# Optimization experiments

Measured on AMD Instinct MI355X. Metric: run time of the kernel, lower is better.

## Reference

```python
import jax, jax.numpy as jnp
import numpy as np

N, NFEAT, NHID, NCLASS, NHEADS = 50000, 512, 256, 64, 8
C1 = NHID // NHEADS  # 32 per-head channels, layer 1
NEG_SLOPE = 0.2


def setup_inputs() -> dict:
    key = jax.random.key(0)
    ks = jax.random.split(key, 10)
    x = jax.random.normal(ks[0], (N, NFEAT), dtype=jnp.float32)
    edge_idx = jax.random.randint(ks[1], (2, 800000), 0, N, dtype=jnp.int64)
    s = 0.05
    return {
        "x": x,
        "edge_idx": edge_idx,
        "W1": jax.random.normal(ks[2], (NFEAT, NHEADS, C1), dtype=jnp.float32) * s,
        "a1_src": jax.random.normal(ks[3], (NHEADS, C1), dtype=jnp.float32) * s,
        "a1_dst": jax.random.normal(ks[4], (NHEADS, C1), dtype=jnp.float32) * s,
        "b1": jnp.zeros((NHID,), dtype=jnp.float32),
        "W2": jax.random.normal(ks[5], (NHID, NHEADS, NCLASS), dtype=jnp.float32) * s,
        "a2_src": jax.random.normal(ks[6], (NHEADS, NCLASS), dtype=jnp.float32) * s,
        "a2_dst": jax.random.normal(ks[7], (NHEADS, NCLASS), dtype=jnp.float32) * s,
        "b2": jnp.zeros((NCLASS,), dtype=jnp.float32),
    }


def gat_conv(x, src, dst, W, a_src, a_dst, b, concat):
    # x: [N, F_in]; W: [F_in, H, C]; a_*: [H, C]; src/dst: [E]
    h = jnp.einsum("nf,fhc->nhc", x, W)             # [N, H, C]
    e_src = jnp.sum(h * a_src, axis=-1)              # [N, H]
    e_dst = jnp.sum(h * a_dst, axis=-1)              # [N, H]
    alpha = e_src[src] + e_dst[dst]                  # [E, H]
    alpha = jnp.where(alpha > 0, alpha, NEG_SLOPE * alpha)  # leaky_relu(0.2)
    # segment softmax over incoming edges of each destination node
    m = jax.ops.segment_max(alpha, dst, num_segments=N)     # [N, H]
    m = jnp.where(jnp.isfinite(m), m, 0.0)
    e = jnp.exp(alpha - m[dst])                      # [E, H]
    z = jax.ops.segment_sum(e, dst, num_segments=N)  # [N, H]
    coef = e / z[dst]                                # [E, H]
    msg = h[src] * coef[:, :, None]                  # [E, H, C]
    out = jax.ops.segment_sum(msg, dst, num_segments=N)  # [N, H, C]
    if concat:
        out = out.reshape(N, -1)
    else:
        out = out.mean(axis=1)
    return out + b


def reference(x, edge_idx, W1, a1_src, a1_dst, b1, W2, a2_src, a2_dst, b2):
    # add self loops (PyG GATConv default)
    loop = jnp.arange(N, dtype=edge_idx.dtype)
    src = jnp.concatenate([edge_idx[0], loop])
    dst = jnp.concatenate([edge_idx[1], loop])
    h = gat_conv(x, src, dst, W1, a1_src, a1_dst, b1, concat=True)   # [N, NHID]
    h = jax.nn.relu(h)
    # dropout inactive (eval mode)
    out = gat_conv(h, src, dst, W2, a2_src, a2_dst, b2, concat=False)  # [N, NCLASS]
    return jax.nn.log_softmax(out, axis=1)
```

## Files before the change

kernel.cpp:

```cpp
#include <hip/hip_runtime.h>
#include <math.h>

#define NN 50000
#define NF 512
#define NHID 256
#define NCLASS 64
#define NHEADS 8

typedef __attribute__((ext_vector_type(8))) short bf16x8;
typedef __attribute__((ext_vector_type(4))) float f32x4;
typedef __attribute__((ext_vector_type(2))) float f32x2;
typedef __attribute__((ext_vector_type(4))) unsigned int u32x4;
typedef __attribute__((ext_vector_type(2))) unsigned int u32x2;

static __device__ __forceinline__ unsigned short f2bf(float f) {
  unsigned int u = __float_as_uint(f);
  unsigned int r = (u + 0x7fffu + ((u >> 16) & 1u)) >> 16;
  return (unsigned short)r;
}
static __device__ __forceinline__ float bf2f(unsigned short u) {
  return __uint_as_float(((unsigned int)u) << 16);
}
static __device__ __forceinline__ float2 bfpair(unsigned int u) {
  return make_float2(__uint_as_float(u << 16), __uint_as_float(u & 0xffff0000u));
}

static __device__ __forceinline__ u32x4 gld128(const void* p) {
  u32x4 r;
  asm volatile("global_load_dwordx4 %0, %1, off"
               : "=v"(r) : "v"((unsigned long long)p));
  return r;
}
static __device__ __forceinline__ u32x2 gld64(const void* p) {
  u32x2 r;
  asm volatile("global_load_dwordx2 %0, %1, off"
               : "=v"(r) : "v"((unsigned long long)p));
  return r;
}
static __device__ __forceinline__ int gld32i(const void* p) {
  int r;
  asm volatile("global_load_dword %0, %1, off"
               : "=v"(r) : "v"((unsigned long long)p));
  return r;
}
static __device__ __forceinline__ float gld32f(const void* p) {
  float r;
  asm volatile("global_load_dword %0, %1, off"
               : "=v"(r) : "v"((unsigned long long)p));
  return r;
}
#define VMCNT0()                                        \
  do {                                                  \
    asm volatile("s_waitcnt vmcnt(0)" ::: "memory");    \
    __builtin_amdgcn_sched_barrier(0);                  \
  } while (0)

__global__ void k_init_deg(int* deg) {
  int i = blockIdx.x * blockDim.x + threadIdx.x;
  if (i < NN) deg[i] = 1;
}

__global__ void k_count(const int* __restrict__ dst, int E0, int* deg) {
  int i = blockIdx.x * blockDim.x + threadIdx.x;
  if (i < E0) atomicAdd(&deg[dst[i]], 1);
}

__global__ __launch_bounds__(1024) void k_scan(const int* __restrict__ deg, int* offs,
                                               int* cursor) {
  __shared__ int wbase[16];
  __shared__ int srun;
  int tid = threadIdx.x;
  int lane = tid & 63;
  int wv = tid >> 6;
  if (tid == 0) srun = 0;
  __syncthreads();
  for (int base = 0; base < NN; base += 4096) {
    int i = base + tid * 4;
    int4 v;
    if (i + 3 < NN) {
      v = *(const int4*)(deg + i);
    } else {
      v.x = (i + 0 < NN) ? deg[i + 0] : 0;
      v.y = (i + 1 < NN) ? deg[i + 1] : 0;
      v.z = (i + 2 < NN) ? deg[i + 2] : 0;
      v.w = (i + 3 < NN) ? deg[i + 3] : 0;
    }
    int tot = v.x + v.y + v.z + v.w;
    int s = tot;
    #pragma unroll
    for (int o = 1; o < 64; o <<= 1) {
      int t = __shfl_up(s, o);
      if (lane >= o) s += t;
    }
    if (lane == 63) wbase[wv] = s;
    __syncthreads();
    if (tid == 0) {
      int run = srun;
      #pragma unroll
      for (int w2 = 0; w2 < 16; w2++) {
        int t = wbase[w2];
        wbase[w2] = run;
        run += t;
      }
      srun = run;
    }
    __syncthreads();
    int p = wbase[wv] + s - tot;
    if (i + 0 < NN) { offs[i + 0] = p; cursor[i + 0] = p; p += v.x; }
    if (i + 1 < NN) { offs[i + 1] = p; cursor[i + 1] = p; p += v.y; }
    if (i + 2 < NN) { offs[i + 2] = p; cursor[i + 2] = p; p += v.z; }
    if (i + 3 < NN) { offs[i + 3] = p; cursor[i + 3] = p; }
  }
  __syncthreads();
  if (tid == 0) offs[NN] = srun;
}

__global__ void k_scatter(const int* __restrict__ src, const int* __restrict__ dst,
                          int E0, int* cursor, int* __restrict__ nbr) {
  int i = blockIdx.x * blockDim.x + threadIdx.x;
  if (i < E0) {
    int pos = atomicAdd(&cursor[dst[i]], 1);
    nbr[pos] = src[i];
  } else if (i < E0 + NN) {
    int v = i - E0;
    int pos = atomicAdd(&cursor[v], 1);
    nbr[pos] = v;
  }
}

__global__ void k_cast4(const float* __restrict__ in, unsigned short* __restrict__ out,
                        int n4) {
  int i = blockIdx.x * blockDim.x + threadIdx.x;
  if (i >= n4) return;
  float4 v = *(const float4*)(in + (size_t)i * 4);
  ushort4 o;
  o.x = f2bf(v.x); o.y = f2bf(v.y); o.z = f2bf(v.z); o.w = f2bf(v.w);
  *(ushort4*)(out + (size_t)i * 4) = o;
}

__global__ void k_castWt(const float* __restrict__ W, unsigned short* __restrict__ Wt,
                         int K, int cols) {
  int i = blockIdx.x * blockDim.x + threadIdx.x;
  if (i >= K * cols) return;
  int k = i / cols, c = i % cols;
  Wt[(size_t)c * K + k] = f2bf(W[i]);
}

__global__ void k_castWt_perm(const float* __restrict__ W, unsigned short* __restrict__ Wt,
                              int K) {
  int i = blockIdx.x * blockDim.x + threadIdx.x;
  if (i >= K * NHEADS * NCLASS) return;
  int k = i / (NHEADS * NCLASS);
  int rem = i % (NHEADS * NCLASS);
  int h = rem / NCLASS, c = rem % NCLASS;
  Wt[(size_t)(c * NHEADS + h) * K + k] = f2bf(W[i]);
}

__global__ void k_cast_fp8(const unsigned short* __restrict__ in,
                           unsigned char* __restrict__ out, int n8) {
  int i = blockIdx.x * blockDim.x + threadIdx.x;
  if (i >= n8) return;
  uint4 raw = *(const uint4*)(in + (size_t)i * 8);
  float2 p0 = bfpair(raw.x), p1 = bfpair(raw.y), p2 = bfpair(raw.z), p3 = bfpair(raw.w);
  int lo = 0, hi = 0;
  lo = __builtin_amdgcn_cvt_pk_fp8_f32(p0.x, p0.y, lo, false);
  lo = __builtin_amdgcn_cvt_pk_fp8_f32(p1.x, p1.y, lo, true);
  hi = __builtin_amdgcn_cvt_pk_fp8_f32(p2.x, p2.y, hi, false);
  hi = __builtin_amdgcn_cvt_pk_fp8_f32(p3.x, p3.y, hi, true);
  u32x2 o; o[0] = (unsigned int)lo; o[1] = (unsigned int)hi;
  *(u32x2*)(out + (size_t)i * 8) = o;
}

__global__ __launch_bounds__(256) void k_gemm_bf(const unsigned short* __restrict__ A,
                                                 const unsigned short* __restrict__ Bt,
                                                 unsigned short* __restrict__ C,
                                                 int rows, int K, int cols) {
  __shared__ unsigned short Bs[256 * 40];
  int t = threadIdx.x;
  int wave = t >> 6, lane = t & 63;
  int quad = lane >> 4, sixt = lane & 15;
  int rb = blockIdx.x * 64 + (wave >> 1) * 32;
  int cw = (wave & 1) * 128;
  int cbw = blockIdx.y * 256 + cw;
  int r0 = rb + sixt, r1 = rb + 16 + sixt;
  const unsigned short* Ap0 = A + (size_t)(r0 < rows ? r0 : 0) * K + quad * 8;
  const unsigned short* Ap1 = A + (size_t)(r1 < rows ? r1 : 0) * K + quad * 8;
  const unsigned short* Bg = Bt + (size_t)(blockIdx.y * 256 + (t >> 2)) * K + (t & 3) * 8;
  const size_t BgStep = (size_t)64 * K;
  char* BsW = (char*)Bs + (t >> 2) * 80 + (t & 3) * 16;
  f32x4 acc0[8] = {}, acc1[8] = {};
  for (int k0 = 0; k0 < K; k0 += 32) {
    uint4 v0 = *(const uint4*)(Bg + k0);
    uint4 v1 = *(const uint4*)(Bg + BgStep + k0);
    uint4 v2 = *(const uint4*)(Bg + 2 * BgStep + k0);
    uint4 v3 = *(const uint4*)(Bg + 3 * BgStep + k0);
    bf16x8 a0 = *(const bf16x8*)(Ap0 + k0);
    bf16x8 a1 = *(const bf16x8*)(Ap1 + k0);
    *(uint4*)(BsW) = v0;
    *(uint4*)(BsW + 64 * 80) = v1;
    *(uint4*)(BsW + 128 * 80) = v2;
    *(uint4*)(BsW + 192 * 80) = v3;
    __syncthreads();
    #pragma unroll
    for (int g = 0; g < 8; g++) {
      bf16x8 b = *(const bf16x8*)((const char*)Bs + (cw + g * 16 + sixt) * 80 + quad * 16);
      acc0[g] = __builtin_amdgcn_mfma_f32_16x16x32_bf16(a0, b, acc0[g], 0, 0, 0);
      acc1[g] = __builtin_amdgcn_mfma_f32_16x16x32_bf16(a1, b, acc1[g], 0, 0, 0);
    }
    __syncthreads();
  }
  #pragma unroll
  for (int r = 0; r < 4; r++) {
    int row = rb + quad * 4 + r;
    if (row < rows) {
      unsigned short* out = C + (size_t)row * cols + cbw + sixt;
      #pragma unroll
      for (int g = 0; g < 8; g++) out[g * 16] = f2bf(acc0[g][r]);
    }
    int row2 = row + 16;
    if (row2 < rows) {
      unsigned short* out = C + (size_t)row2 * cols + cbw + sixt;
      #pragma unroll
      for (int g = 0; g < 8; g++) out[g * 16] = f2bf(acc1[g][r]);
    }
  }
}

template <int C>
__global__ void k_escore_c(const unsigned short* __restrict__ h,
                           const float* __restrict__ asr, const float* __restrict__ ads,
                           float* __restrict__ es, float* __restrict__ ed) {
  int idx = blockIdx.x * blockDim.x + threadIdx.x;
  if (idx >= NN * NHEADS) return;
  int hd = idx & 7;
  const unsigned short* row = h + (size_t)idx * C;
  float s = 0.f, d = 0.f;
  #pragma unroll
  for (int c8 = 0; c8 < C / 8; c8++) {
    uint4 raw = *(const uint4*)(row + c8 * 8);
    float2 p0 = bfpair(raw.x), p1 = bfpair(raw.y), p2 = bfpair(raw.z), p3 = bfpair(raw.w);
    const float* as_ = asr + hd * C + c8 * 8;
    const float* ad_ = ads + hd * C + c8 * 8;
    s += p0.x * as_[0] + p0.y * as_[1] + p1.x * as_[2] + p1.y * as_[3] +
         p2.x * as_[4] + p2.y * as_[5] + p3.x * as_[6] + p3.y * as_[7];
    d += p0.x * ad_[0] + p0.y * ad_[1] + p1.x * ad_[2] + p1.y * ad_[3] +
         p2.x * ad_[4] + p2.y * ad_[5] + p3.x * ad_[6] + p3.y * ad_[7];
  }
  es[idx] = s;
  ed[idx] = d;
}

__global__ void k_escore_p(const unsigned short* __restrict__ h,
                           const float* __restrict__ asr, const float* __restrict__ ads,
                           float* __restrict__ es, float* __restrict__ ed) {
  int idx = blockIdx.x * blockDim.x + threadIdx.x;
  if (idx >= NN * NHEADS) return;
  int hd = idx & 7;
  int n = idx >> 3;
  const unsigned short* row = h + (size_t)n * (NHEADS * NCLASS) + hd;
  float s = 0.f, d = 0.f;
  #pragma unroll
  for (int c = 0; c < NCLASS; c++) {
    float v = bf2f(row[c * NHEADS]);
    s += v * asr[hd * NCLASS + c];
    d += v * ads[hd * NCLASS + c];
  }
  es[idx] = s;
  ed[idx] = d;
}

__global__ __launch_bounds__(256) void k_agg1f(const int* __restrict__ offs,
                                               const int* __restrict__ nbr,
                                               const unsigned short* __restrict__ h1,
                                               const float* __restrict__ es,
                                               const float* __restrict__ ed,
                                               const float* __restrict__ b1,
                                               unsigned short* __restrict__ out) {
  int node = blockIdx.x * 4 + (threadIdx.x >> 6);
  if (node >= NN) return;
  int lane = threadIdx.x & 63;
  int h = lane & 7;
  int sub = lane >> 3;
  int col = lane << 2;
  int beg = offs[node], end = offs[node + 1];
  float edst = ed[node * NHEADS + h];
  int kb = beg;
  int iA = kb + (lane & 7); if (iA > end - 1) iA = end - 1;
  int vt = gld32i(nbr + iA);
  int vtN = 0;
  if (kb + 8 < end) {
    int iB = kb + 8 + (lane & 7); if (iB > end - 1) iB = end - 1;
    vtN = gld32i(nbr + iB);
  }
  VMCNT0();
  int se[8];
  #pragma unroll
  for (int e = 0; e < 8; e++) se[e] = __shfl(vt, e);
  float esv;
  {
    int sv = __shfl(vt, sub);
    esv = gld32f(es + (size_t)sv * NHEADS + h);
  }
  VMCNT0();
  float m = -1e30f, z = 0.f;
  float4 acc = make_float4(0.f, 0.f, 0.f, 0.f);
  while (true) {
    int cnt = end - kb; if (cnt > 8) cnt = 8;
    u32x2 r[8];
    #pragma unroll
    for (int e = 0; e < 8; e++)
      if (e < cnt) r[e] = gld64(h1 + (size_t)se[e] * NHID + col);
    bool more = kb + 8 < end, more2 = kb + 16 < end;
    int vt2 = 0;
    if (more2) {
      int iC = kb + 16 + (lane & 7); if (iC > end - 1) iC = end - 1;
      vt2 = gld32i(nbr + iC);
    }
    float esvN = 0.f;
    if (more) {
      int svN = __shfl(vtN, sub);
      esvN = gld32f(es + (size_t)svN * NHEADS + h);
    }
    float ar = esv + edst;
    ar = (ar > 0.f) ? ar : 0.2f * ar;
    float a = (kb + sub < end) ? ar : -1e30f;
    float gm = a;
    #pragma unroll
    for (int o = 8; o < 64; o <<= 1) gm = fmaxf(gm, __shfl_xor(gm, o));
    float mn = fmaxf(m, gm);
    float ee = __expf(a - mn);
    float zg = ee;
    #pragma unroll
    for (int o = 8; o < 64; o <<= 1) zg += __shfl_xor(zg, o);
    float sc = __expf(m - mn);
    z = z * sc + zg;
    m = mn;
    VMCNT0();
    float sch = __shfl(sc, sub);
    acc.x *= sch; acc.y *= sch; acc.z *= sch; acc.w *= sch;
    #pragma unroll
    for (int e = 0; e < 8; e++) {
      if (e < cnt) {
        float ce = __shfl(ee, e * 8 + sub);
        float2 p0 = bfpair(r[e][0]), p1 = bfpair(r[e][1]);
        acc.x += ce * p0.x;
        acc.y += ce * p0.y;
        acc.z += ce * p1.x;
        acc.w += ce * p1.y;
      }
    }
    if (!more) break;
    kb += 8;
    #pragma unroll
    for (int e = 0; e < 8; e++) se[e] = __shfl(vtN, e);
    esv = esvN;
    vtN = vt2;
  }
  float inv = 1.f / z;
  float ivh = __shfl(inv, sub);
  ushort4 o;
  o.x = f2bf(fmaxf(acc.x * ivh + b1[col + 0], 0.f));
  o.y = f2bf(fmaxf(acc.y * ivh + b1[col + 1], 0.f));
  o.z = f2bf(fmaxf(acc.z * ivh + b1[col + 2], 0.f));
  o.w = f2bf(fmaxf(acc.w * ivh + b1[col + 3], 0.f));
  *(ushort4*)(out + (size_t)node * NHID + col) = o;
}

__global__ __launch_bounds__(256) void k_agg2f(const int* __restrict__ offs,
                                               const int* __restrict__ nbr,
                                               const unsigned char* __restrict__ h2f8,
                                               const float* __restrict__ es,
                                               const float* __restrict__ ed,
                                               const float* __restrict__ b2,
                                               float* __restrict__ out) {
  __shared__ __align__(16) float cs[4][64];
  int wv = threadIdx.x >> 6;
  int node = blockIdx.x * 4 + wv;
  if (node >= NN) return;
  int lane = threadIdx.x & 63;
  int h = lane & 7;
  int sub = lane >> 3;
  int beg = offs[node], end = offs[node + 1];
  float edst = ed[node * NHEADS + h];
  int kb = beg;
  int iA = kb + (lane & 7); if (iA > end - 1) iA = end - 1;
  int vt = gld32i(nbr + iA);
  int vtN = 0;
  if (kb + 8 < end) {
    int iB = kb + 8 + (lane & 7); if (iB > end - 1) iB = end - 1;
    vtN = gld32i(nbr + iB);
  }
  VMCNT0();
  int se[8];
  #pragma unroll
  for (int e = 0; e < 8; e++) se[e] = __shfl(vt, e);
  float esv;
  {
    int sv = __shfl(vt, sub);
    esv = gld32f(es + (size_t)sv * NHEADS + h);
  }
  VMCNT0();
  float m = -1e30f, z = 0.f;
  float acc[8] = {};
  while (true) {
    int cnt = end - kb; if (cnt > 8) cnt = 8;
    u32x2 r[8];
    #pragma unroll
    for (int e = 0; e < 8; e++)
      if (e < cnt) r[e] = gld64(h2f8 + (size_t)se[e] * (NHEADS * NCLASS) + (lane << 3));
    bool more = kb + 8 < end, more2 = kb + 16 < end;
    int vt2 = 0;
    if (more2) {
      int iC = kb + 16 + (lane & 7); if (iC > end - 1) iC = end - 1;
      vt2 = gld32i(nbr + iC);
    }
    float esvN = 0.f;
    if (more) {
      int svN = __shfl(vtN, sub);
      esvN = gld32f(es + (size_t)svN * NHEADS + h);
    }
    float ar = esv + edst;
    ar = (ar > 0.f) ? ar : 0.2f * ar;
    float a = (kb + sub < end) ? ar : -1e30f;
    float gm = a;
    #pragma unroll
    for (int o = 8; o < 64; o <<= 1) gm = fmaxf(gm, __shfl_xor(gm, o));
    float mn = fmaxf(m, gm);
    float ee = __expf(a - mn);
    float zg = ee;
    #pragma unroll
    for (int o = 8; o < 64; o <<= 1) zg += __shfl_xor(zg, o);
    float sc = __expf(m - mn);
    z = z * sc + zg;
    m = mn;
    cs[wv][lane] = ee;
    VMCNT0();
    #pragma unroll
    for (int hh = 0; hh < 8; hh++) acc[hh] *= __shfl(sc, hh);
    #pragma unroll
    for (int e = 0; e < 8; e++) {
      if (e < cnt) {
        float4 cA = *(const float4*)&cs[wv][e * 8];
        float4 cB = *(const float4*)&cs[wv][e * 8 + 4];
        f32x2 q0 = __builtin_amdgcn_cvt_pk_f32_fp8((int)r[e][0], false);
        f32x2 q1 = __builtin_amdgcn_cvt_pk_f32_fp8((int)r[e][0], true);
        f32x2 q2 = __builtin_amdgcn_cvt_pk_f32_fp8((int)r[e][1], false);
        f32x2 q3 = __builtin_amdgcn_cvt_pk_f32_fp8((int)r[e][1], true);
        acc[0] += cA.x * q0.x;
        acc[1] += cA.y * q0.y;
        acc[2] += cA.z * q1.x;
        acc[3] += cA.w * q1.y;
        acc[4] += cB.x * q2.x;
        acc[5] += cB.y * q2.y;
        acc[6] += cB.z * q3.x;
        acc[7] += cB.w * q3.y;
      }
    }
    if (!more) break;
    kb += 8;
    #pragma unroll
    for (int e = 0; e < 8; e++) se[e] = __shfl(vtN, e);
    esv = esvN;
    vtN = vt2;
  }
  float inv = 1.f / z;
  float val = 0.f;
  #pragma unroll
  for (int hh = 0; hh < 8; hh++) val += acc[hh] * __shfl(inv, hh);
  val = val * 0.125f + b2[lane];
  float mx = val;
  #pragma unroll
  for (int o = 32; o > 0; o >>= 1) mx = fmaxf(mx, __shfl_xor(mx, o));
  float ex = __expf(val - mx);
  float sm = ex;
  #pragma unroll
  for (int o = 32; o > 0; o >>= 1) sm += __shfl_xor(sm, o);
  out[(size_t)node * NCLASS + lane] = val - mx - __logf(sm);
}

extern "C" void kernel_launch(void* const* d_in, const int* in_sizes, int n_in,
                              void* d_out, int out_size, void* d_ws, size_t ws_size,
                              hipStream_t stream) {
  const float* x   = (const float*)d_in[0];
  const int* eidx  = (const int*)d_in[1];
  const float* W1  = (const float*)d_in[2];
  const float* a1s = (const float*)d_in[3];
  const float* a1d = (const float*)d_in[4];
  const float* b1  = (const float*)d_in[5];
  const float* W2  = (const float*)d_in[6];
  const float* a2s = (const float*)d_in[7];
  const float* a2d = (const float*)d_in[8];
  const float* b2  = (const float*)d_in[9];
  const int E0 = in_sizes[1] / 2;
  const int* esrc = eidx;
  const int* edst = eidx + E0;
  const int E = E0 + NN;

  char* w = (char*)d_ws;
  auto carve = [&](size_t bytes) {
    void* p = (void*)w;
    w += (bytes + 255) & ~(size_t)255;
    return p;
  };
  int* deg      = (int*)carve((size_t)NN * 4);
  int* offs     = (int*)carve((size_t)(NN + 1) * 4);
  int* cursor   = (int*)carve((size_t)NN * 4);
  int* nbr      = (int*)carve((size_t)E * 4);
  float* es1    = (float*)carve((size_t)NN * NHEADS * 4);
  float* ed1    = (float*)carve((size_t)NN * NHEADS * 4);
  unsigned short* xbf   = (unsigned short*)carve((size_t)NN * NF * 2);
  unsigned short* W1t   = (unsigned short*)carve((size_t)NF * NHID * 2);
  unsigned short* W2t   = (unsigned short*)carve((size_t)NHID * NHEADS * NCLASS * 2);
  unsigned short* h1b   = (unsigned short*)carve((size_t)NN * NHID * 2);
  unsigned short* out1b = (unsigned short*)carve((size_t)NN * NHID * 2);
  unsigned short* h2b   = (unsigned short*)carve((size_t)NN * NHEADS * NCLASS * 2);
  unsigned char* h2f8 = (unsigned char*)xbf;

  k_init_deg<<<(NN + 255) / 256, 256, 0, stream>>>(deg);
  k_count<<<(E0 + 255) / 256, 256, 0, stream>>>(edst, E0, deg);
  k_scan<<<1, 1024, 0, stream>>>(deg, offs, cursor);
  k_scatter<<<(E0 + NN + 255) / 256, 256, 0, stream>>>(esrc, edst, E0, cursor, nbr);

  k_cast4<<<(NN * NF / 4 + 255) / 256, 256, 0, stream>>>(x, xbf, NN * NF / 4);
  k_castWt<<<(NF * NHID + 255) / 256, 256, 0, stream>>>(W1, W1t, NF, NHID);
  k_castWt_perm<<<(NHID * NHEADS * NCLASS + 255) / 256, 256, 0, stream>>>(W2, W2t, NHID);

  k_gemm_bf<<<dim3((NN + 63) / 64, NHID / 256), 256, 0, stream>>>(xbf, W1t, h1b,
                                                                  NN, NF, NHID);
  k_escore_c<32><<<(NN * NHEADS + 255) / 256, 256, 0, stream>>>(h1b, a1s, a1d, es1, ed1);
  k_agg1f<<<(NN + 3) / 4, 256, 0, stream>>>(offs, nbr, h1b, es1, ed1, b1, out1b);

  k_gemm_bf<<<dim3((NN + 63) / 64, (NHEADS * NCLASS) / 256), 256, 0, stream>>>(
      out1b, W2t, h2b, NN, NHID, NHEADS * NCLASS);
  k_escore_p<<<(NN * NHEADS + 255) / 256, 256, 0, stream>>>(h2b, a2s, a2d, es1, ed1);
  k_cast_fp8<<<(NN * NHEADS * NCLASS / 8 + 255) / 256, 256, 0, stream>>>(
      h2b, h2f8, NN * NHEADS * NCLASS / 8);
  k_agg2f<<<(NN + 3) / 4, 256, 0, stream>>>(offs, nbr, h2f8, es1, ed1, b2,
                                            (float*)d_out);
}
```

Measured before the change: 571.0 us.

## Use FP8 features for layer-1 gather and emit FP8 directly from layer-2 GEMM

Layer-1 features are cast to FP8 before the neighbor aggregation, which halves the bytes gathered per edge in k_agg1f. The layer-2 GEMM now writes FP8 output directly through a new kernel. That removes the bf16 h2 buffer and the separate cast pass, and the score kernel now reads FP8. In exchange it adds one cast kernel for layer 1 and loses precision in both aggregations, which could hurt accuracy tolerance.

Result: faster. 548.0 us (-4.0%).

```diff
diff --git a/kernel.cpp b/kernel.cpp
--- a/kernel.cpp
+++ b/kernel.cpp
@@ -25,12 +25,6 @@
   return make_float2(__uint_as_float(u << 16), __uint_as_float(u & 0xffff0000u));
 }
 
-static __device__ __forceinline__ u32x4 gld128(const void* p) {
-  u32x4 r;
-  asm volatile("global_load_dwordx4 %0, %1, off"
-               : "=v"(r) : "v"((unsigned long long)p));
-  return r;
-}
 static __device__ __forceinline__ u32x2 gld64(const void* p) {
   u32x2 r;
   asm volatile("global_load_dwordx2 %0, %1, off"
@@ -226,6 +220,67 @@
   }
 }
 
+__global__ __launch_bounds__(256) void k_gemm_bf8(const unsigned short* __restrict__ A,
+                                                  const unsigned short* __restrict__ Bt,
+                                                  unsigned char* __restrict__ C,
+                                                  int rows, int K, int cols) {
+  __shared__ unsigned short Bs[256 * 40];
+  int t = threadIdx.x;
+  int wave = t >> 6, lane = t & 63;
+  int quad = lane >> 4, sixt = lane & 15;
+  int rb = blockIdx.x * 64 + (wave >> 1) * 32;
+  int cw = (wave & 1) * 128;
+  int cbw = blockIdx.y * 256 + cw;
+  int r0 = rb + sixt, r1 = rb + 16 + sixt;
+  const unsigned short* Ap0 = A + (size_t)(r0 < rows ? r0 : 0) * K + quad * 8;
+  const unsigned short* Ap1 = A + (size_t)(r1 < rows ? r1 : 0) * K + quad * 8;
+  const unsigned short* Bg = Bt + (size_t)(blockIdx.y * 256 + (t >> 2)) * K + (t & 3) * 8;
+  const size_t BgStep = (size_t)64 * K;
+  char* BsW = (char*)Bs + (t >> 2) * 80 + (t & 3) * 16;
+  f32x4 acc0[8] = {}, acc1[8] = {};
+  for (int k0 = 0; k0 < K; k0 += 32) {
+    uint4 v0 = *(const uint4*)(Bg + k0);
+    uint4 v1 = *(const uint4*)(Bg + BgStep + k0);
+    uint4 v2 = *(const uint4*)(Bg + 2 * BgStep + k0);
+    uint4 v3 = *(const uint4*)(Bg + 3 * BgStep + k0);
+    bf16x8 a0 = *(const bf16x8*)(Ap0 + k0);
+    bf16x8 a1 = *(const bf16x8*)(Ap1 + k0);
+    *(uint4*)(BsW) = v0;
+    *(uint4*)(BsW + 64 * 80) = v1;
+    *(uint4*)(BsW + 128 * 80) = v2;
+    *(uint4*)(BsW + 192 * 80) = v3;
+    __syncthreads();
+    #pragma unroll
+    for (int g = 0; g < 8; g++) {
+      bf16x8 b = *(const bf16x8*)((const char*)Bs + (cw + g * 16 + sixt) * 80 + quad * 16);
+      acc0[g] = __builtin_amdgcn_mfma_f32_16x16x32_bf16(a0, b, acc0[g], 0, 0, 0);
+      acc1[g] = __builtin_amdgcn_mfma_f32_16x16x32_bf16(a1, b, acc1[g], 0, 0, 0);
+    }
+    __syncthreads();
+  }
+  #pragma unroll
+  for (int r = 0; r < 4; r++) {
+    int row = rb + quad * 4 + r;
+    if (row < rows) {
+      unsigned char* out = C + (size_t)row * cols + cbw + sixt;
+      #pragma unroll
+      for (int g = 0; g < 8; g++) {
+        int wq = __builtin_amdgcn_cvt_pk_fp8_f32(acc0[g][r], acc0[g][r], 0, false);
+        out[g * 16] = (unsigned char)(wq & 0xff);
+      }
+    }
+    int row2 = row + 16;
+    if (row2 < rows) {
+      unsigned char* out = C + (size_t)row2 * cols + cbw + sixt;
+      #pragma unroll
+      for (int g = 0; g < 8; g++) {
+        int wq = __builtin_amdgcn_cvt_pk_fp8_f32(acc1[g][r], acc1[g][r], 0, false);
+        out[g * 16] = (unsigned char)(wq & 0xff);
+      }
+    }
+  }
+}
+
 template <int C>
 __global__ void k_escore_c(const unsigned short* __restrict__ h,
                            const float* __restrict__ asr, const float* __restrict__ ads,
@@ -250,18 +305,22 @@
   ed[idx] = d;
 }
 
-__global__ void k_escore_p(const unsigned short* __restrict__ h,
-                           const float* __restrict__ asr, const float* __restrict__ ads,
-                           float* __restrict__ es, float* __restrict__ ed) {
+__global__ void k_escore_p8(const unsigned char* __restrict__ h,
+                            const float* __restrict__ asr, const float* __restrict__ ads,
+                            float* __restrict__ es, float* __restrict__ ed) {
   int idx = blockIdx.x * blockDim.x + threadIdx.x;
   if (idx >= NN * NHEADS) return;
   int hd = idx & 7;
   int n = idx >> 3;
-  const unsigned short* row = h + (size_t)n * (NHEADS * NCLASS) + hd;
+  const unsigned short* rp =
+      (const unsigned short*)(h + (size_t)n * (NHEADS * NCLASS) + (hd & ~1));
+  int hi = hd & 1;
   float s = 0.f, d = 0.f;
   #pragma unroll
   for (int c = 0; c < NCLASS; c++) {
-    float v = bf2f(row[c * NHEADS]);
+    unsigned short w = rp[c * 4];
+    f32x2 q = __builtin_amdgcn_cvt_pk_f32_fp8((int)w, false);
+    float v = hi ? q.y : q.x;
     s += v * asr[hd * NCLASS + c];
     d += v * ads[hd * NCLASS + c];
   }
@@ -271,7 +330,7 @@
 
 __global__ __launch_bounds__(256) void k_agg1f(const int* __restrict__ offs,
                                                const int* __restrict__ nbr,
-                                               const unsigned short* __restrict__ h1,
+                                               const unsigned char* __restrict__ h1f8,
                                                const float* __restrict__ es,
                                                const float* __restrict__ ed,
                                                const float* __restrict__ b1,
@@ -306,10 +365,10 @@
   float4 acc = make_float4(0.f, 0.f, 0.f, 0.f);
   while (true) {
     int cnt = end - kb; if (cnt > 8) cnt = 8;
-    u32x2 r[8];
+    int r[8];
     #pragma unroll
     for (int e = 0; e < 8; e++)
-      if (e < cnt) r[e] = gld64(h1 + (size_t)se[e] * NHID + col);
+      if (e < cnt) r[e] = gld32i(h1f8 + (size_t)se[e] * NHID + col);
     bool more = kb + 8 < end, more2 = kb + 16 < end;
     int vt2 = 0;
     if (more2) {
@@ -342,11 +401,12 @@
     for (int e = 0; e < 8; e++) {
       if (e < cnt) {
         float ce = __shfl(ee, e * 8 + sub);
-        float2 p0 = bfpair(r[e][0]), p1 = bfpair(r[e][1]);
-        acc.x += ce * p0.x;
-        acc.y += ce * p0.y;
-        acc.z += ce * p1.x;
-        acc.w += ce * p1.y;
+        f32x2 q0 = __builtin_amdgcn_cvt_pk_f32_fp8(r[e], false);
+        f32x2 q1 = __builtin_amdgcn_cvt_pk_f32_fp8(r[e], true);
+        acc.x += ce * q0.x;
+        acc.y += ce * q0.y;
+        acc.z += ce * q1.x;
+        acc.w += ce * q1.y;
       }
     }
     if (!more) break;
@@ -513,7 +573,7 @@
   unsigned short* W2t   = (unsigned short*)carve((size_t)NHID * NHEADS * NCLASS * 2);
   unsigned short* h1b   = (unsigned short*)carve((size_t)NN * NHID * 2);
   unsigned short* out1b = (unsigned short*)carve((size_t)NN * NHID * 2);
-  unsigned short* h2b   = (unsigned short*)carve((size_t)NN * NHEADS * NCLASS * 2);
+  unsigned char* h1f8   = (unsigned char*)carve((size_t)NN * NHID);
   unsigned char* h2f8 = (unsigned char*)xbf;
 
   k_init_deg<<<(NN + 255) / 256, 256, 0, stream>>>(deg);
@@ -528,13 +588,12 @@
   k_gemm_bf<<<dim3((NN + 63) / 64, NHID / 256), 256, 0, stream>>>(xbf, W1t, h1b,
                                                                   NN, NF, NHID);
   k_escore_c<32><<<(NN * NHEADS + 255) / 256, 256, 0, stream>>>(h1b, a1s, a1d, es1, ed1);
-  k_agg1f<<<(NN + 3) / 4, 256, 0, stream>>>(offs, nbr, h1b, es1, ed1, b1, out1b);
-
-  k_gemm_bf<<<dim3((NN + 63) / 64, (NHEADS * NCLASS) / 256), 256, 0, stream>>>(
-      out1b, W2t, h2b, NN, NHID, NHEADS * NCLASS);
-  k_escore_p<<<(NN * NHEADS + 255) / 256, 256, 0, stream>>>(h2b, a2s, a2d, es1, ed1);
-  k_cast_fp8<<<(NN * NHEADS * NCLASS / 8 + 255) / 256, 256, 0, stream>>>(
-      h2b, h2f8, NN * NHEADS * NCLASS / 8);
+  k_cast_fp8<<<(NN * NHID / 8 + 255) / 256, 256, 0, stream>>>(h1b, h1f8, NN * NHID / 8);
+  k_agg1f<<<(NN + 3) / 4, 256, 0, stream>>>(offs, nbr, h1f8, es1, ed1, b1, out1b);
+
+  k_gemm_bf8<<<dim3((NN + 63) / 64, (NHEADS * NCLASS) / 256), 256, 0, stream>>>(
+      out1b, W2t, h2f8, NN, NHID, NHEADS * NCLASS);
+  k_escore_p8<<<(NN * NHEADS + 255) / 256, 256, 0, stream>>>(h2f8, a2s, a2d, es1, ed1);
   k_agg2f<<<(NN + 3) / 4, 256, 0, stream>>>(offs, nbr, h2f8, es1, ed1, b2,
                                             (float*)d_out);
 }
```
